# Performance work log

Hardware: AMD Instinct MI355X
Metric: run time of the kernel (lower is better)

Reference implementation:

```python
import jax, jax.numpy as jnp
import numpy as np

N_NODES = 100000
N_EDGES = 1600000
F_IN = 256
EMB = 16  # conv1 out = 2*EMB = 32, conv2 out = EMB


def setup_inputs() -> dict:
    key = jax.random.key(0)
    k1, k2, k3, k4, k5, k6, k7 = jax.random.split(key, 7)
    x = jax.random.normal(k1, (N_NODES, F_IN), dtype=jnp.float32)
    edge_index = jax.random.randint(k2, (2, N_EDGES), 0, N_NODES, dtype=jnp.int64)
    edge_weight = jax.random.uniform(k3, (N_EDGES,), dtype=jnp.float32)
    # GCNConv params: glorot-ish weights, zero bias (materialized as params)
    s1 = 1.0 / np.sqrt(F_IN)
    s2 = 1.0 / np.sqrt(2 * EMB)
    W1 = jax.random.uniform(k4, (F_IN, 2 * EMB), minval=-s1, maxval=s1, dtype=jnp.float32)
    b1 = jnp.zeros((2 * EMB,), dtype=jnp.float32)
    W2 = jax.random.uniform(k5, (2 * EMB, EMB), minval=-s2, maxval=s2, dtype=jnp.float32)
    b2 = jnp.zeros((EMB,), dtype=jnp.float32)
    return {"x": x, "edge_index": edge_index, "edge_weight": edge_weight,
            "W1": W1, "b1": b1, "W2": W2, "b2": b2}


def _gcn_norm(edge_index, edge_weight, num_nodes, dtype):
    # PyG gcn_norm with add_self_loops=True, fill_value=1.0
    row, col = edge_index[0], edge_index[1]
    loop = jnp.arange(num_nodes)
    row_a = jnp.concatenate([row, loop])
    col_a = jnp.concatenate([col, loop])
    w_a = jnp.concatenate([edge_weight, jnp.ones((num_nodes,), dtype=dtype)])
    deg = jax.ops.segment_sum(w_a, col_a, num_segments=num_nodes)
    dinv = jnp.where(deg > 0, jax.lax.rsqrt(deg), jnp.zeros_like(deg))
    norm = dinv[row_a] * w_a * dinv[col_a]
    return row_a, col_a, norm


def _gcn_conv(x, W, b, row, col, norm, num_nodes):
    h = x @ W                                  # [N, d_out] dense projection
    msg = norm[:, None] * h[row]               # gather + edge scale, [E+N, d_out]
    out = jax.ops.segment_sum(msg, col, num_segments=num_nodes)  # scatter-add
    return out + b


def reference(x, edge_index, edge_weight, W1, b1, W2, b2):
    n = x.shape[0]
    row, col, norm = _gcn_norm(edge_index, edge_weight, n, x.dtype)
    h = jax.nn.relu(_gcn_conv(x, W1, b1, row, col, norm, n))
    return _gcn_conv(h, W2, b2, row, col, norm, n)
```

## Files before the change

### kernel.cpp

```cpp
#include <hip/hip_runtime.h>
#include <hip/hip_bf16.h>

#define NN   100000
#define NE   1600000
#define FIN  256
#define HID  32
#define OUTD 16
#define NBLK ((NN + 255) / 256)
#define GEMM_BLOCKS ((NN + 127) / 128)
#define CNT_BLOCKS  ((NE + 255) / 256)
#define FUSE_BLOCKS (GEMM_BLOCKS + CNT_BLOCKS)

#define OFF_FLAG    0
#define OFF_DEGPACK 64
#define OFF_DINV    (OFF_DEGPACK + 2*NN)
#define OFF_RANK    (OFF_DINV + NN)
#define OFF_BSUM    (OFF_RANK + NE)
#define OFF_BOFF    (OFF_BSUM + 512)
#define OFF_ROWPTR  (OFF_BOFF + 512)
#define OFF_CSR     (OFF_ROWPTR + NN + 32)
#define OFF_H1      (OFF_CSR + 2*NE)
#define OFF_P2      (OFF_H1 + NN*HID)

#define PACK_SHIFT 40
#define PACK_MASK  ((1ull << PACK_SHIFT) - 1ull)
#define FP_SCALE   16777216.0f
#define FP_INV     (1.0f / 16777216.0f)

__device__ __forceinline__ float bf2f(unsigned short u) {
  union { unsigned int i; float f; } v; v.i = ((unsigned int)u) << 16; return v.f;
}
__device__ __forceinline__ unsigned short f2bf(float f) {
  union { float f; unsigned int i; } v; v.f = f;
  unsigned int x = v.i;
  return (unsigned short)((x + 0x7fffu + ((x >> 16) & 1u)) >> 16);
}
__device__ __forceinline__ int eidx(const int* __restrict__ ei, long long pos, int is64) {
  return is64 ? ei[2 * pos] : ei[pos];
}
__device__ __forceinline__ float ldf(const void* p, long long i, int isf32) {
  return isf32 ? ((const float*)p)[i] : bf2f(((const unsigned short*)p)[i]);
}

__global__ __launch_bounds__(256) void detect_zero_kernel(const int* __restrict__ ei,
    const unsigned short* __restrict__ xu, int* __restrict__ flags,
    float* __restrict__ zp, int zn) {
  int b = blockIdx.x;
  if (b == 0) {
    __shared__ int any, cnt;
    if (threadIdx.x == 0) { any = 0; cnt = 0; }
    __syncthreads();
    int local = 0, c = 0;
    for (int i = threadIdx.x; i < 2048; i += 256) local |= ei[2 * i + 1];
    for (int i = threadIdx.x; i < 1024; i += 256) {
      unsigned int e = (xu[2 * i] >> 7) & 0xFF;
      c += (e < 100 || e > 140) ? 1 : 0;
    }
    if (local) atomicOr(&any, 1);
    atomicAdd(&cnt, c);
    __syncthreads();
    if (threadIdx.x == 0) {
      flags[0] = (any == 0) ? 1 : 0;
      flags[1] = (cnt > 100) ? 1 : 0;
    }
  } else {
    int stride = (gridDim.x - 1) * 256;
    for (int i = (b - 1) * 256 + threadIdx.x; i < zn; i += stride) zp[i] = 0.f;
  }
}

__global__ __launch_bounds__(256) void count_gemm_kernel(const int* __restrict__ ei,
    const void* __restrict__ ew, unsigned long long* __restrict__ degpack,
    int* __restrict__ rank, const void* __restrict__ x,
    const void* __restrict__ W1, float* __restrict__ h1,
    const int* __restrict__ flags) {
  __shared__ float wlds[FIN][HID];
  __shared__ float xs[32][132];
  int b = blockIdx.x;
  int t = threadIdx.x;
  bool is_gemm = ((b % 9) == 0) && (b / 9) < GEMM_BLOCKS;

  if (!is_gemm) {
    int cid = b - 1 - b / 9;
    int e = cid * 256 + t;
    if (e >= NE) return;
    int c = eidx(ei, (long long)NE + e, flags[0]);
    float w = ldf(ew, e, flags[1]);
    unsigned long long inc = (1ull << PACK_SHIFT)
                           | (unsigned long long)(w * FP_SCALE + 0.5f);
    unsigned long long old = atomicAdd(degpack + c, inc);
    rank[e] = (int)(old >> PACK_SHIFT);
    return;
  }

  int rb = (b / 9) * 128;
  int isf32 = flags[1];

  if (isf32) {
    const float* wrow = (const float*)W1 + t * HID;
    #pragma unroll
    for (int jj = 0; jj < HID; jj += 4)
      *(float4*)&wlds[t][jj] = *((const float4*)(wrow + jj));
  } else {
    const unsigned short* wrow = (const unsigned short*)W1 + t * HID;
    #pragma unroll
    for (int jj = 0; jj < HID; jj += 8) {
      uint4 pk = *((const uint4*)(wrow + jj));
      const unsigned short* pu = (const unsigned short*)&pk;
      #pragma unroll
      for (int q = 0; q < 8; q++) wlds[t][jj + q] = bf2f(pu[q]);
    }
  }

  int j0 = (t & 15) * 2;
  int r0 = (t >> 4) * 8;
  float acc[8][2];
  #pragma unroll
  for (int i = 0; i < 8; i++) { acc[i][0] = 0.f; acc[i][1] = 0.f; }

  for (int kc = 0; kc < FIN; kc += 32) {
    __syncthreads();
    {
      int rr = t >> 1;
      int kk0 = (t & 1) * 16;
      int grow = rb + rr;
      if (grow < NN) {
        if (isf32) {
          const float* xp = (const float*)x + (long long)grow * FIN + kc + kk0;
          #pragma unroll
          for (int q4 = 0; q4 < 4; q4++) {
            float4 p = ((const float4*)xp)[q4];
            xs[kk0 + q4 * 4 + 0][rr] = p.x;
            xs[kk0 + q4 * 4 + 1][rr] = p.y;
            xs[kk0 + q4 * 4 + 2][rr] = p.z;
            xs[kk0 + q4 * 4 + 3][rr] = p.w;
          }
        } else {
          const unsigned short* xp = (const unsigned short*)x + (long long)grow * FIN + kc + kk0;
          uint4 p0 = ((const uint4*)xp)[0];
          uint4 p1 = ((const uint4*)xp)[1];
          const unsigned short* pu = (const unsigned short*)&p0;
          #pragma unroll
          for (int q = 0; q < 8; q++) xs[kk0 + q][rr] = bf2f(pu[q]);
          pu = (const unsigned short*)&p1;
          #pragma unroll
          for (int q = 0; q < 8; q++) xs[kk0 + 8 + q][rr] = bf2f(pu[q]);
        }
      } else {
        #pragma unroll
        for (int q = 0; q < 16; q++) xs[kk0 + q][rr] = 0.f;
      }
    }
    __syncthreads();
    #pragma unroll 8
    for (int kk = 0; kk < 32; kk++) {
      float w0 = wlds[kc + kk][j0];
      float w1 = wlds[kc + kk][j0 + 1];
      const float4* xr = (const float4*)&xs[kk][r0];
      float4 xa = xr[0], xb = xr[1];
      float xv[8] = {xa.x, xa.y, xa.z, xa.w, xb.x, xb.y, xb.z, xb.w};
      #pragma unroll
      for (int i = 0; i < 8; i++) {
        acc[i][0] = fmaf(xv[i], w0, acc[i][0]);
        acc[i][1] = fmaf(xv[i], w1, acc[i][1]);
      }
    }
  }
  #pragma unroll
  for (int i = 0; i < 8; i++) {
    int grow = rb + r0 + i;
    if (grow < NN) {
      float2 v; v.x = acc[i][0]; v.y = acc[i][1];
      *((float2*)(h1 + (long long)grow * HID + j0)) = v;
    }
  }
}

__global__ __launch_bounds__(256) void dinv_scansum_kernel(
    const unsigned long long* __restrict__ degpack, float* __restrict__ dinv,
    int* __restrict__ bsum) {
  int b = blockIdx.x;
  if (b < NBLK) {
    __shared__ int s[256];
    int i = b * 256 + threadIdx.x;
    s[threadIdx.x] = (i < NN) ? (int)(degpack[i] >> PACK_SHIFT) : 0;
    __syncthreads();
    for (int off = 128; off > 0; off >>= 1) {
      if (threadIdx.x < off) s[threadIdx.x] += s[threadIdx.x + off];
      __syncthreads();
    }
    if (threadIdx.x == 0) bsum[b] = s[0];
  } else {
    int i = (b - NBLK) * 256 + threadIdx.x;
    if (i >= NN) return;
    float d = (float)(degpack[i] & PACK_MASK) * FP_INV + 1.0f;
    dinv[i] = (d > 0.f) ? rsqrtf(d) : 0.f;
  }
}

__global__ __launch_bounds__(512) void scan_offs_kernel(const int* __restrict__ bsum,
                                                        int* __restrict__ boff) {
  __shared__ int a[512];
  int t = threadIdx.x;
  int orig = (t < NBLK) ? bsum[t] : 0;
  a[t] = orig;
  __syncthreads();
  for (int off = 1; off < 512; off <<= 1) {
    int v = a[t] + ((t >= off) ? a[t - off] : 0);
    __syncthreads();
    a[t] = v;
    __syncthreads();
  }
  if (t < NBLK) boff[t] = a[t] - orig;
}

__global__ __launch_bounds__(256) void scan_write_kernel(const unsigned long long* __restrict__ degpack,
    const int* __restrict__ boff, int* __restrict__ rowptr) {
  __shared__ int a[256];
  int t = threadIdx.x;
  int i = blockIdx.x * 256 + t;
  int orig = (i < NN) ? (int)(degpack[i] >> PACK_SHIFT) : 0;
  a[t] = orig;
  __syncthreads();
  for (int off = 1; off < 256; off <<= 1) {
    int v = a[t] + ((t >= off) ? a[t - off] : 0);
    __syncthreads();
    a[t] = v;
    __syncthreads();
  }
  if (i < NN) rowptr[i] = boff[blockIdx.x] + a[t] - orig;
  if (blockIdx.x == 0 && t == 0) rowptr[NN] = NE;
}

__global__ __launch_bounds__(256) void fill_csr_kernel(const int* __restrict__ ei,
    const void* __restrict__ ew, const float* __restrict__ dinv,
    const int* __restrict__ rowptr, const int* __restrict__ rank,
    int2* __restrict__ csr, const int* __restrict__ flags) {
  int e = blockIdx.x * 256 + threadIdx.x;
  if (e >= NE) return;
  int is64 = flags[0];
  int r = eidx(ei, e, is64);
  int c = eidx(ei, (long long)NE + e, is64);
  float nw = dinv[r] * ldf(ew, e, flags[1]) * dinv[c];
  int pos = rowptr[c] + rank[e];
  int2 pr; pr.x = r; pr.y = __float_as_int(nw);
  csr[pos] = pr;
}

__global__ __launch_bounds__(256) void gather1_kernel(const float* __restrict__ h1,
    const float* __restrict__ dinv, const int* __restrict__ rowptr,
    const int2* __restrict__ csr, const void* __restrict__ b1,
    const void* __restrict__ W2, float* __restrict__ p2,
    const int* __restrict__ flags) {
  __shared__ float w2lds[HID * OUTD];
  __shared__ float b1l[HID];
  __shared__ float tl[8][HID + 1];
  int t = threadIdx.x;
  int isf32 = flags[1];
  w2lds[2 * t]     = ldf(W2, 2 * t, isf32);
  w2lds[2 * t + 1] = ldf(W2, 2 * t + 1, isf32);
  if (t < HID) b1l[t] = ldf(b1, t, isf32);
  __syncthreads();

  int nl = t >> 5;
  int j  = t & 31;
  int node = blockIdx.x * 8 + nl;
  if (node < NN) {
    int k0 = rowptr[node], k1 = rowptr[node + 1];
    float acc = 0.f;
    int k = k0;
    for (; k + 8 <= k1; k += 8) {
      int2 q0 = csr[k];     int2 q1 = csr[k + 1];
      int2 q2 = csr[k + 2]; int2 q3 = csr[k + 3];
      int2 q4 = csr[k + 4]; int2 q5 = csr[k + 5];
      int2 q6 = csr[k + 6]; int2 q7 = csr[k + 7];
      float v0 = h1[q0.x * HID + j]; float v1 = h1[q1.x * HID + j];
      float v2 = h1[q2.x * HID + j]; float v3 = h1[q3.x * HID + j];
      float v4 = h1[q4.x * HID + j]; float v5 = h1[q5.x * HID + j];
      float v6 = h1[q6.x * HID + j]; float v7 = h1[q7.x * HID + j];
      acc = fmaf(__int_as_float(q0.y), v0, acc);
      acc = fmaf(__int_as_float(q1.y), v1, acc);
      acc = fmaf(__int_as_float(q2.y), v2, acc);
      acc = fmaf(__int_as_float(q3.y), v3, acc);
      acc = fmaf(__int_as_float(q4.y), v4, acc);
      acc = fmaf(__int_as_float(q5.y), v5, acc);
      acc = fmaf(__int_as_float(q6.y), v6, acc);
      acc = fmaf(__int_as_float(q7.y), v7, acc);
    }
    for (; k + 4 <= k1; k += 4) {
      int2 q0 = csr[k];     int2 q1 = csr[k + 1];
      int2 q2 = csr[k + 2]; int2 q3 = csr[k + 3];
      float v0 = h1[q0.x * HID + j]; float v1 = h1[q1.x * HID + j];
      float v2 = h1[q2.x * HID + j]; float v3 = h1[q3.x * HID + j];
      acc = fmaf(__int_as_float(q0.y), v0, acc);
      acc = fmaf(__int_as_float(q1.y), v1, acc);
      acc = fmaf(__int_as_float(q2.y), v2, acc);
      acc = fmaf(__int_as_float(q3.y), v3, acc);
    }
    for (; k < k1; k++) {
      int2 pr = csr[k];
      acc = fmaf(__int_as_float(pr.y), h1[pr.x * HID + j], acc);
    }
    float di = dinv[node];
    acc = fmaf(di * di, h1[node * HID + j], acc);
    acc += b1l[j];
    tl[nl][j] = fmaxf(acc, 0.f);
  }
  __syncthreads();
  int m = t & 31;
  if (node < NN && m < OUTD) {
    float s = 0.f;
    #pragma unroll
    for (int k = 0; k < HID; k++) s = fmaf(tl[nl][k], w2lds[k * OUTD + m], s);
    p2[node * OUTD + m] = s;
  }
}

__global__ __launch_bounds__(256) void gather2_kernel(const float* __restrict__ p2,
    const float* __restrict__ dinv, const int* __restrict__ rowptr,
    const int2* __restrict__ csr, const void* __restrict__ b2,
    void* __restrict__ out, const int* __restrict__ flags) {
  __shared__ float b2l[OUTD];
  int t = threadIdx.x;
  int isf32 = flags[1];
  if (t < OUTD) b2l[t] = ldf(b2, t, isf32);
  __syncthreads();

  int nl = t >> 4;
  int m  = t & 15;
  int node = blockIdx.x * 16 + nl;
  if (node >= NN) return;
  int k0 = rowptr[node], k1 = rowptr[node + 1];
  float acc = 0.f;
  int k = k0;
  for (; k + 8 <= k1; k += 8) {
    int2 q0 = csr[k];     int2 q1 = csr[k + 1];
    int2 q2 = csr[k + 2]; int2 q3 = csr[k + 3];
    int2 q4 = csr[k + 4]; int2 q5 = csr[k + 5];
    int2 q6 = csr[k + 6]; int2 q7 = csr[k + 7];
    float v0 = p2[q0.x * OUTD + m]; float v1 = p2[q1.x * OUTD + m];
    float v2 = p2[q2.x * OUTD + m]; float v3 = p2[q3.x * OUTD + m];
    float v4 = p2[q4.x * OUTD + m]; float v5 = p2[q5.x * OUTD + m];
    float v6 = p2[q6.x * OUTD + m]; float v7 = p2[q7.x * OUTD + m];
    acc = fmaf(__int_as_float(q0.y), v0, acc);
    acc = fmaf(__int_as_float(q1.y), v1, acc);
    acc = fmaf(__int_as_float(q2.y), v2, acc);
    acc = fmaf(__int_as_float(q3.y), v3, acc);
    acc = fmaf(__int_as_float(q4.y), v4, acc);
    acc = fmaf(__int_as_float(q5.y), v5, acc);
    acc = fmaf(__int_as_float(q6.y), v6, acc);
    acc = fmaf(__int_as_float(q7.y), v7, acc);
  }
  for (; k + 4 <= k1; k += 4) {
    int2 q0 = csr[k];     int2 q1 = csr[k + 1];
    int2 q2 = csr[k + 2]; int2 q3 = csr[k + 3];
    float v0 = p2[q0.x * OUTD + m]; float v1 = p2[q1.x * OUTD + m];
    float v2 = p2[q2.x * OUTD + m]; float v3 = p2[q3.x * OUTD + m];
    acc = fmaf(__int_as_float(q0.y), v0, acc);
    acc = fmaf(__int_as_float(q1.y), v1, acc);
    acc = fmaf(__int_as_float(q2.y), v2, acc);
    acc = fmaf(__int_as_float(q3.y), v3, acc);
  }
  for (; k < k1; k++) {
    int2 pr = csr[k];
    acc = fmaf(__int_as_float(pr.y), p2[pr.x * OUTD + m], acc);
  }
  float di = dinv[node];
  acc = fmaf(di * di, p2[node * OUTD + m], acc);
  acc += b2l[m];
  int oidx = node * OUTD + m;
  if (isf32) ((float*)out)[oidx] = acc;
  else       ((unsigned short*)out)[oidx] = f2bf(acc);
}

extern "C" void kernel_launch(void* const* d_in, const int* in_sizes, int n_in,
                              void* d_out, int out_size, void* d_ws, size_t ws_size,
                              hipStream_t stream) {
  const void* x  = d_in[0];
  const int* ei  = (const int*)d_in[1];
  const void* ew = d_in[2];
  const void* W1 = d_in[3];
  const void* b1 = d_in[4];
  const void* W2 = d_in[5];
  const void* b2 = d_in[6];
  float* ws = (float*)d_ws;
  int* wsi = (int*)d_ws;
  unsigned long long* degpack = (unsigned long long*)(wsi + OFF_DEGPACK);

  detect_zero_kernel<<<dim3(513), dim3(256), 0, stream>>>(ei, (const unsigned short*)x,
      wsi + OFF_FLAG, ws + OFF_DEGPACK, 2 * NN);
  count_gemm_kernel<<<dim3(FUSE_BLOCKS), dim3(256), 0, stream>>>(ei, ew, degpack,
      wsi + OFF_RANK, x, W1, ws + OFF_H1, wsi + OFF_FLAG);
  dinv_scansum_kernel<<<dim3(2 * NBLK), dim3(256), 0, stream>>>(degpack, ws + OFF_DINV, wsi + OFF_BSUM);
  scan_offs_kernel<<<dim3(1), dim3(512), 0, stream>>>(wsi + OFF_BSUM, wsi + OFF_BOFF);
  scan_write_kernel<<<dim3(NBLK), dim3(256), 0, stream>>>(degpack, wsi + OFF_BOFF, wsi + OFF_ROWPTR);
  fill_csr_kernel<<<dim3((NE + 255) / 256), dim3(256), 0, stream>>>(ei, ew, ws + OFF_DINV, wsi + OFF_ROWPTR, wsi + OFF_RANK, (int2*)(wsi + OFF_CSR), wsi + OFF_FLAG);
  gather1_kernel<<<dim3((NN + 7) / 8), dim3(256), 0, stream>>>(ws + OFF_H1, ws + OFF_DINV, wsi + OFF_ROWPTR, (const int2*)(wsi + OFF_CSR), b1, W2, ws + OFF_P2, wsi + OFF_FLAG);
  gather2_kernel<<<dim3((NN + 15) / 16), dim3(256), 0, stream>>>(ws + OFF_P2, ws + OFF_DINV, wsi + OFF_ROWPTR, (const int2*)(wsi + OFF_CSR), b2, d_out, wsi + OFF_FLAG);
}
```

Measured before the change: 365.5 us.

## Retile GEMM with register prefetch, batch edge work, fold scan offsets

```diff
diff --git a/kernel.cpp b/kernel.cpp
--- a/kernel.cpp
+++ b/kernel.cpp
@@ -7,9 +7,13 @@
 #define HID  32
 #define OUTD 16
 #define NBLK ((NN + 255) / 256)
-#define GEMM_BLOCKS ((NN + 127) / 128)
-#define CNT_BLOCKS  ((NE + 255) / 256)
+
+#define GEMM_ROWS   64
+#define GEMM_BLOCKS ((NN + GEMM_ROWS - 1) / GEMM_ROWS)
+#define CNT_EDGES   2048
+#define CNT_BLOCKS  ((NE + CNT_EDGES - 1) / CNT_EDGES)
 #define FUSE_BLOCKS (GEMM_BLOCKS + CNT_BLOCKS)
+#define FILL_BLOCKS ((NE + 1023) / 1024)
 
 #define OFF_FLAG    0
 #define OFF_DEGPACK 64
@@ -74,33 +78,48 @@
     int* __restrict__ rank, const void* __restrict__ x,
     const void* __restrict__ W1, float* __restrict__ h1,
     const int* __restrict__ flags) {
-  __shared__ float wlds[FIN][HID];
-  __shared__ float xs[32][132];
+  __shared__ float wlds[FIN * HID];
+  __shared__ float xs[32][GEMM_ROWS];
   int b = blockIdx.x;
   int t = threadIdx.x;
-  bool is_gemm = ((b % 9) == 0) && (b / 9) < GEMM_BLOCKS;
-
-  if (!is_gemm) {
-    int cid = b - 1 - b / 9;
-    int e = cid * 256 + t;
-    if (e >= NE) return;
-    int c = eidx(ei, (long long)NE + e, flags[0]);
-    float w = ldf(ew, e, flags[1]);
-    unsigned long long inc = (1ull << PACK_SHIFT)
-                           | (unsigned long long)(w * FP_SCALE + 0.5f);
-    unsigned long long old = atomicAdd(degpack + c, inc);
-    rank[e] = (int)(old >> PACK_SHIFT);
+
+  if ((b % 3) == 0) {
+    int cid = b / 3;
+    int is64 = flags[0], isf32 = flags[1];
+    int e0 = cid * CNT_EDGES + t;
+    int c[8]; float w[8];
+    #pragma unroll
+    for (int q = 0; q < 8; q++) {
+      int e = e0 + q * 256;
+      if (e < NE) {
+        c[q] = eidx(ei, (long long)NE + e, is64);
+        w[q] = ldf(ew, e, isf32);
+      } else c[q] = -1;
+    }
+    unsigned long long old[8];
+    #pragma unroll
+    for (int q = 0; q < 8; q++) {
+      if (c[q] >= 0) {
+        unsigned long long inc = (1ull << PACK_SHIFT)
+                               | (unsigned long long)(w[q] * FP_SCALE + 0.5f);
+        old[q] = atomicAdd(degpack + c[q], inc);
+      }
+    }
+    #pragma unroll
+    for (int q = 0; q < 8; q++)
+      if (c[q] >= 0) rank[e0 + q * 256] = (int)(old[q] >> PACK_SHIFT);
     return;
   }
 
-  int rb = (b / 9) * 128;
+  int gid = b - b / 3 - 1;
+  int rb = gid * GEMM_ROWS;
   int isf32 = flags[1];
 
   if (isf32) {
     const float* wrow = (const float*)W1 + t * HID;
     #pragma unroll
     for (int jj = 0; jj < HID; jj += 4)
-      *(float4*)&wlds[t][jj] = *((const float4*)(wrow + jj));
+      *(float4*)&wlds[t * HID + jj] = *((const float4*)(wrow + jj));
   } else {
     const unsigned short* wrow = (const unsigned short*)W1 + t * HID;
     #pragma unroll
@@ -108,70 +127,77 @@
       uint4 pk = *((const uint4*)(wrow + jj));
       const unsigned short* pu = (const unsigned short*)&pk;
       #pragma unroll
-      for (int q = 0; q < 8; q++) wlds[t][jj + q] = bf2f(pu[q]);
+      for (int q = 0; q < 8; q++) wlds[t * HID + jj + q] = bf2f(pu[q]);
     }
   }
 
   int j0 = (t & 15) * 2;
-  int r0 = (t >> 4) * 8;
-  float acc[8][2];
+  int r0 = (t >> 4) * 4;
+  int rr  = t >> 2;
+  int kk0 = (t & 3) * 8;
+  int grow = rb + rr;
+  float acc[4][2];
   #pragma unroll
-  for (int i = 0; i < 8; i++) { acc[i][0] = 0.f; acc[i][1] = 0.f; }
+  for (int i = 0; i < 4; i++) { acc[i][0] = 0.f; acc[i][1] = 0.f; }
+
+  union { uint4 u[2]; float f[8]; } pf;
+
+  {
+    if (grow < NN) {
+      if (isf32) {
+        const float* xp = (const float*)x + (long long)grow * FIN + kk0;
+        pf.u[0] = ((const uint4*)xp)[0];
+        pf.u[1] = ((const uint4*)xp)[1];
+      } else {
+        const unsigned short* xp = (const unsigned short*)x + (long long)grow * FIN + kk0;
+        pf.u[0] = *(const uint4*)xp;
+      }
+    } else { pf.u[0] = make_uint4(0,0,0,0); pf.u[1] = make_uint4(0,0,0,0); }
+  }
 
   for (int kc = 0; kc < FIN; kc += 32) {
     __syncthreads();
-    {
-      int rr = t >> 1;
-      int kk0 = (t & 1) * 16;
-      int grow = rb + rr;
+    if (isf32) {
+      #pragma unroll
+      for (int q = 0; q < 8; q++) xs[kk0 + q][rr] = pf.f[q];
+    } else {
+      const unsigned short* pu = (const unsigned short*)&pf.u[0];
+      #pragma unroll
+      for (int q = 0; q < 8; q++) xs[kk0 + q][rr] = bf2f(pu[q]);
+    }
+    __syncthreads();
+    if (kc + 32 < FIN) {
       if (grow < NN) {
         if (isf32) {
-          const float* xp = (const float*)x + (long long)grow * FIN + kc + kk0;
-          #pragma unroll
-          for (int q4 = 0; q4 < 4; q4++) {
-            float4 p = ((const float4*)xp)[q4];
-            xs[kk0 + q4 * 4 + 0][rr] = p.x;
-            xs[kk0 + q4 * 4 + 1][rr] = p.y;
-            xs[kk0 + q4 * 4 + 2][rr] = p.z;
-            xs[kk0 + q4 * 4 + 3][rr] = p.w;
-          }
+          const float* xp = (const float*)x + (long long)grow * FIN + kc + 32 + kk0;
+          pf.u[0] = ((const uint4*)xp)[0];
+          pf.u[1] = ((const uint4*)xp)[1];
         } else {
-          const unsigned short* xp = (const unsigned short*)x + (long long)grow * FIN + kc + kk0;
-          uint4 p0 = ((const uint4*)xp)[0];
-          uint4 p1 = ((const uint4*)xp)[1];
-          const unsigned short* pu = (const unsigned short*)&p0;
-          #pragma unroll
-          for (int q = 0; q < 8; q++) xs[kk0 + q][rr] = bf2f(pu[q]);
-          pu = (const unsigned short*)&p1;
-          #pragma unroll
-          for (int q = 0; q < 8; q++) xs[kk0 + 8 + q][rr] = bf2f(pu[q]);
+          const unsigned short* xp = (const unsigned short*)x + (long long)grow * FIN + kc + 32 + kk0;
+          pf.u[0] = *(const uint4*)xp;
         }
-      } else {
-        #pragma unroll
-        for (int q = 0; q < 16; q++) xs[kk0 + q][rr] = 0.f;
       }
     }
-    __syncthreads();
     #pragma unroll 8
     for (int kk = 0; kk < 32; kk++) {
-      float w0 = wlds[kc + kk][j0];
-      float w1 = wlds[kc + kk][j0 + 1];
-      const float4* xr = (const float4*)&xs[kk][r0];
-      float4 xa = xr[0], xb = xr[1];
-      float xv[8] = {xa.x, xa.y, xa.z, xa.w, xb.x, xb.y, xb.z, xb.w};
-      #pragma unroll
-      for (int i = 0; i < 8; i++) {
-        acc[i][0] = fmaf(xv[i], w0, acc[i][0]);
-        acc[i][1] = fmaf(xv[i], w1, acc[i][1]);
-      }
+      float2 wp = *(const float2*)&wlds[(kc + kk) * HID + j0];
+      float4 xv = *(const float4*)&xs[kk][r0];
+      acc[0][0] = fmaf(xv.x, wp.x, acc[0][0]);
+      acc[0][1] = fmaf(xv.x, wp.y, acc[0][1]);
+      acc[1][0] = fmaf(xv.y, wp.x, acc[1][0]);
+      acc[1][1] = fmaf(xv.y, wp.y, acc[1][1]);
+      acc[2][0] = fmaf(xv.z, wp.x, acc[2][0]);
+      acc[2][1] = fmaf(xv.z, wp.y, acc[2][1]);
+      acc[3][0] = fmaf(xv.w, wp.x, acc[3][0]);
+      acc[3][1] = fmaf(xv.w, wp.y, acc[3][1]);
     }
   }
   #pragma unroll
-  for (int i = 0; i < 8; i++) {
-    int grow = rb + r0 + i;
-    if (grow < NN) {
+  for (int i = 0; i < 4; i++) {
+    int gr = rb + r0 + i;
+    if (gr < NN) {
       float2 v; v.x = acc[i][0]; v.y = acc[i][1];
-      *((float2*)(h1 + (long long)grow * HID + j0)) = v;
+      *((float2*)(h1 + (long long)gr * HID + j0)) = v;
     }
   }
 }
@@ -198,53 +224,70 @@
   }
 }
 
-__global__ __launch_bounds__(512) void scan_offs_kernel(const int* __restrict__ bsum,
-                                                        int* __restrict__ boff) {
-  __shared__ int a[512];
+__global__ __launch_bounds__(256) void scan_write_kernel(const unsigned long long* __restrict__ degpack,
+    const int* __restrict__ bsum, int* __restrict__ rowptr) {
+  __shared__ int a[256];
+  __shared__ int base_s;
   int t = threadIdx.x;
-  int orig = (t < NBLK) ? bsum[t] : 0;
-  a[t] = orig;
-  __syncthreads();
-  for (int off = 1; off < 512; off <<= 1) {
-    int v = a[t] + ((t >= off) ? a[t - off] : 0);
-    __syncthreads();
-    a[t] = v;
-    __syncthreads();
-  }
-  if (t < NBLK) boff[t] = a[t] - orig;
-}
-
-__global__ __launch_bounds__(256) void scan_write_kernel(const unsigned long long* __restrict__ degpack,
-    const int* __restrict__ boff, int* __restrict__ rowptr) {
-  __shared__ int a[256];
-  int t = threadIdx.x;
-  int i = blockIdx.x * 256 + t;
+  int b = blockIdx.x;
+  int v = 0;
+  for (int i = t; i < NBLK; i += 256) v += (i < b) ? bsum[i] : 0;
+  a[t] = v;
+  __syncthreads();
+  for (int off = 128; off > 0; off >>= 1) {
+    if (t < off) a[t] += a[t + off];
+    __syncthreads();
+  }
+  if (t == 0) base_s = a[0];
+  __syncthreads();
+  int base = base_s;
+  int i = b * 256 + t;
   int orig = (i < NN) ? (int)(degpack[i] >> PACK_SHIFT) : 0;
   a[t] = orig;
   __syncthreads();
   for (int off = 1; off < 256; off <<= 1) {
-    int v = a[t] + ((t >= off) ? a[t - off] : 0);
-    __syncthreads();
-    a[t] = v;
-    __syncthreads();
-  }
-  if (i < NN) rowptr[i] = boff[blockIdx.x] + a[t] - orig;
-  if (blockIdx.x == 0 && t == 0) rowptr[NN] = NE;
+    int x2 = a[t] + ((t >= off) ? a[t - off] : 0);
+    __syncthreads();
+    a[t] = x2;
+    __syncthreads();
+  }
+  if (i < NN) rowptr[i] = base + a[t] - orig;
+  if (b == 0 && t == 0) rowptr[NN] = NE;
 }
 
 __global__ __launch_bounds__(256) void fill_csr_kernel(const int* __restrict__ ei,
     const void* __restrict__ ew, const float* __restrict__ dinv,
     const int* __restrict__ rowptr, const int* __restrict__ rank,
     int2* __restrict__ csr, const int* __restrict__ flags) {
-  int e = blockIdx.x * 256 + threadIdx.x;
-  if (e >= NE) return;
-  int is64 = flags[0];
-  int r = eidx(ei, e, is64);
-  int c = eidx(ei, (long long)NE + e, is64);
-  float nw = dinv[r] * ldf(ew, e, flags[1]) * dinv[c];
-  int pos = rowptr[c] + rank[e];
-  int2 pr; pr.x = r; pr.y = __float_as_int(nw);
-  csr[pos] = pr;
+  int is64 = flags[0], isf32 = flags[1];
+  int e0 = blockIdx.x * 1024 + threadIdx.x;
+  int r[4], c[4], rk[4]; float w[4];
+  #pragma unroll
+  for (int q = 0; q < 4; q++) {
+    int e = e0 + q * 256;
+    if (e < NE) {
+      r[q]  = eidx(ei, e, is64);
+      c[q]  = eidx(ei, (long long)NE + e, is64);
+      w[q]  = ldf(ew, e, isf32);
+      rk[q] = rank[e];
+    } else c[q] = -1;
+  }
+  float dr[4], dc[4]; int rp[4];
+  #pragma unroll
+  for (int q = 0; q < 4; q++) {
+    if (c[q] >= 0) {
+      dr[q] = dinv[r[q]];
+      dc[q] = dinv[c[q]];
+      rp[q] = rowptr[c[q]];
+    }
+  }
+  #pragma unroll
+  for (int q = 0; q < 4; q++) {
+    if (c[q] >= 0) {
+      int2 pr; pr.x = r[q]; pr.y = __float_as_int(dr[q] * w[q] * dc[q]);
+      csr[rp[q] + rk[q]] = pr;
+    }
+  }
 }
 
 __global__ __launch_bounds__(256) void gather1_kernel(const float* __restrict__ h1,
@@ -392,9 +435,11 @@
   count_gemm_kernel<<<dim3(FUSE_BLOCKS), dim3(256), 0, stream>>>(ei, ew, degpack,
       wsi + OFF_RANK, x, W1, ws + OFF_H1, wsi + OFF_FLAG);
   dinv_scansum_kernel<<<dim3(2 * NBLK), dim3(256), 0, stream>>>(degpack, ws + OFF_DINV, wsi + OFF_BSUM);
-  scan_offs_kernel<<<dim3(1), dim3(512), 0, stream>>>(wsi + OFF_BSUM, wsi + OFF_BOFF);
-  scan_write_kernel<<<dim3(NBLK), dim3(256), 0, stream>>>(degpack, wsi + OFF_BOFF, wsi + OFF_ROWPTR);
-  fill_csr_kernel<<<dim3((NE + 255) / 256), dim3(256), 0, stream>>>(ei, ew, ws + OFF_DINV, wsi + OFF_ROWPTR, wsi + OFF_RANK, (int2*)(wsi + OFF_CSR), wsi + OFF_FLAG);
-  gather1_kernel<<<dim3((NN + 7) / 8), dim3(256), 0, stream>>>(ws + OFF_H1, ws + OFF_DINV, wsi + OFF_ROWPTR, (const int2*)(wsi + OFF_CSR), b1, W2, ws + OFF_P2, wsi + OFF_FLAG);
-  gather2_kernel<<<dim3((NN + 15) / 16), dim3(256), 0, stream>>>(ws + OFF_P2, ws + OFF_DINV, wsi + OFF_ROWPTR, (const int2*)(wsi + OFF_CSR), b2, d_out, wsi + OFF_FLAG);
-}
+  scan_write_kernel<<<dim3(NBLK), dim3(256), 0, stream>>>(degpack, wsi + OFF_BSUM, wsi + OFF_ROWPTR);
+  fill_csr_kernel<<<dim3(FILL_BLOCKS), dim3(256), 0, stream>>>(ei, ew, ws + OFF_DINV,
+      wsi + OFF_ROWPTR, wsi + OFF_RANK, (int2*)(wsi + OFF_CSR), wsi + OFF_FLAG);
+  gather1_kernel<<<dim3((NN + 7) / 8), dim3(256), 0, stream>>>(ws + OFF_H1, ws + OFF_DINV,
+      wsi + OFF_ROWPTR, (const int2*)(wsi + OFF_CSR), b1, W2, ws + OFF_P2, wsi + OFF_FLAG);
+  gather2_kernel<<<dim3((NN + 15) / 16), dim3(256), 0, stream>>>(ws + OFF_P2, ws + OFF_DINV,
+      wsi + OFF_ROWPTR, (const int2*)(wsi + OFF_CSR), b2, d_out, wsi + OFF_FLAG);
+}
```

New measurement: 350.1 us. 1.04x faster.
